# Optimization experiments

Measured on AMD Instinct MI355X. Metric: run time of the kernel, lower is better.

## Reference

```python
import jax, jax.numpy as jnp
import numpy as np

B, L, S = 128, 80, 8          # dialogues, utterances per dialogue, speakers
NODE_DIM, HIDDEN, HEADS, OUT_DIM = 768, 512, 8, 256
N = B * L


def _build_edges():
    """Replicates InterSentenceGNN.build_graph + Batch.from_data_list offsets."""
    rel = np.zeros((N, 3), np.float32)
    all_e, last = [], []
    eye3 = np.eye(3, dtype=np.float32)
    for b in range(B):
        off = b * L
        u = L - 1
        e, t = [], []
        for i in range(L):
            if i > 0:
                e += [[i - 1, i], [i, i - 1]]; t += [0, 0]   # REL_SEQ
            if i < u:
                e += [[i, u], [u, i]]; t += [1, 1]           # REL_CTX
        for s in range(S):                                   # REL_SPK, round-robin speakers
            g = list(range(s, L, S))
            for a in range(len(g)):
                for c in range(a + 1, len(g)):
                    e += [[g[a], g[c]], [g[c], g[a]]]; t += [2, 2]
        e = np.asarray(e, np.int64); t = np.asarray(t, np.int64)
        np.add.at(rel, e[:, 0] + off, eye3[t])               # out-degree per relation (pre-unique)
        all_e.append(np.unique(e, axis=0) + off)             # torch.unique(idx, dim=1)
        last.append(off + u)
    edge_index = np.concatenate(all_e, 0).T.astype(np.int32)  # [2, E], row0=src, row1=dst
    return edge_index, rel, np.asarray(last, np.int32)


def setup_inputs() -> dict:
    key = jax.random.key(0)
    ks = jax.random.split(key, 16)
    edge_index, rel_feat, last_idx = _build_edges()
    g = lambda k, shp, fan: jax.random.normal(k, shp, jnp.float32) * (1.0 / np.sqrt(fan))
    return {
        "x": jax.random.normal(ks[0], (N, NODE_DIM), jnp.float32),
        "rel_feat": jnp.asarray(rel_feat),
        "w1": g(ks[1], (3, 64), 3), "b1": jnp.zeros((64,), jnp.float32),
        "w2": g(ks[2], (64, 1), 64), "b2": jnp.zeros((1,), jnp.float32),
        "Wl1": g(ks[3], (NODE_DIM, HIDDEN), NODE_DIM), "bl1": jnp.zeros((HIDDEN,), jnp.float32),
        "Wr1": g(ks[4], (NODE_DIM, HIDDEN), NODE_DIM), "br1": jnp.zeros((HIDDEN,), jnp.float32),
        "att1": g(ks[5], (HEADS, HIDDEN // HEADS), HIDDEN // HEADS),
        "bias1": jnp.zeros((HIDDEN,), jnp.float32),
        "Wl2": g(ks[6], (HIDDEN, OUT_DIM), HIDDEN), "bl2": jnp.zeros((OUT_DIM,), jnp.float32),
        "Wr2": g(ks[7], (HIDDEN, OUT_DIM), HIDDEN), "br2": jnp.zeros((OUT_DIM,), jnp.float32),
        "att2": g(ks[8], (1, OUT_DIM), OUT_DIM),
        "bias2": jnp.zeros((OUT_DIM,), jnp.float32),
        "ln_g": jnp.ones((OUT_DIM,), jnp.float32), "ln_b": jnp.zeros((OUT_DIM,), jnp.float32),
        "edge_index": jnp.asarray(edge_index),
        "last_idx": jnp.asarray(last_idx),
    }


def _gatv2(x, Wl, bl, Wr, br, att, bias, src, dst, heads, ch, concat):
    """PyG GATv2Conv (eval mode, self-loops already in src/dst)."""
    n = x.shape[0]
    xl = (x @ Wl + bl).reshape(n, heads, ch)   # source transform (messages)
    xr = (x @ Wr + br).reshape(n, heads, ch)   # target transform
    e = jax.nn.leaky_relu(xl[src] + xr[dst], negative_slope=0.2)  # [E,H,C]
    logit = jnp.einsum("ehc,hc->eh", e, att)                      # [E,H]
    m = jax.ops.segment_max(logit, dst, num_segments=n)
    a = jnp.exp(logit - m[dst])
    denom = jax.ops.segment_sum(a, dst, num_segments=n)
    alpha = a / denom[dst]                                        # segment softmax over dst
    msg = (xl[src] * alpha[:, :, None]).reshape(-1, heads * ch)
    out = jax.ops.segment_sum(msg, dst, num_segments=n).reshape(n, heads, ch)
    out = out.reshape(n, heads * ch) if concat else out.mean(axis=1)
    return out + bias


def reference(x, rel_feat, w1, b1, w2, b2, Wl1, bl1, Wr1, br1, att1, bias1,
              Wl2, bl2, Wr2, br2, att2, bias2, ln_g, ln_b, edge_index, last_idx):
    n = x.shape[0]
    loops = jnp.arange(n, dtype=edge_index.dtype)
    src = jnp.concatenate([edge_index[0], loops])  # add_self_loops=True (PyG default)
    dst = jnp.concatenate([edge_index[1], loops])
    w = jax.nn.sigmoid(jax.nn.relu(rel_feat @ w1 + b1) @ w2 + b2)  # [N,1] node gate
    h = x * w
    h = jax.nn.elu(_gatv2(h, Wl1, bl1, Wr1, br1, att1, bias1, src, dst, HEADS, HIDDEN // HEADS, True))
    h = _gatv2(h, Wl2, bl2, Wr2, br2, att2, bias2, src, dst, 1, OUT_DIM, False)
    mu = jnp.mean(h, axis=-1, keepdims=True)
    var = jnp.mean((h - mu) ** 2, axis=-1, keepdims=True)
    h = (h - mu) * jax.lax.rsqrt(var + 1e-5) * ln_g + ln_b
    return h[last_idx]  # x[batch.ptr[1:] - 1]: last (context) node per dialogue
```

## Files before the change

### kernel.cpp

```cpp
#include <hip/hip_runtime.h>
#include <hip/hip_bf16.h>

#define NN 10240
#define LL 80
#define BB 128

typedef _Float16 half8 __attribute__((ext_vector_type(8)));
typedef _Float16 half2v __attribute__((ext_vector_type(2)));
typedef float f32x4 __attribute__((ext_vector_type(4)));

#define GLD16(gptr, lptr)                                                        \
  __builtin_amdgcn_global_load_lds(                                              \
      (const __attribute__((address_space(1))) void*)(gptr),                     \
      (__attribute__((address_space(3))) void*)(lptr), 16, 0, 0)

__device__ __forceinline__ float dot2f(half2v a, half2v b, float c) {
#if __has_builtin(__builtin_amdgcn_fdot2)
  return __builtin_amdgcn_fdot2(a, b, c, false);
#else
  return c + (float)a.x * (float)b.x + (float)a.y * (float)b.y;
#endif
}
__device__ __forceinline__ half2v u2h(unsigned int u) { half2v r; __builtin_memcpy(&r, &u, 4); return r; }
__device__ __forceinline__ unsigned int h2u(half2v h) { unsigned int u; __builtin_memcpy(&u, &h, 4); return u; }
__device__ __forceinline__ unsigned int dupf16(float v) {
  _Float16 hv = (_Float16)v;
  unsigned short u; __builtin_memcpy(&u, &hv, 2);
  return (unsigned int)u * 0x10001u;
}

__global__ __launch_bounds__(256) void prep_all(
    const float* __restrict__ x, const float* __restrict__ rel,
    const float* __restrict__ w1, const float* __restrict__ b1,
    const float* __restrict__ w2, const float* __restrict__ b2,
    const float* __restrict__ Wl1, const float* __restrict__ Wr1,
    const float* __restrict__ Wl2, const float* __restrict__ Wr2,
    const float* __restrict__ bl1, const float* __restrict__ br1,
    const float* __restrict__ att1,
    _Float16* __restrict__ h0, _Float16* __restrict__ Wt1,
    _Float16* __restrict__ Wt2cat,
    float* __restrict__ biasc, _Float16* __restrict__ att_h) {
  __shared__ float tile[32][33];
  int bid = blockIdx.x;
  int tid = threadIdx.x;
  if (bid < NN) {
    int n = bid;
    __shared__ float s_w;
    if (tid < 64) {
      float r0 = rel[n * 3 + 0], r1 = rel[n * 3 + 1], r2 = rel[n * 3 + 2];
      float v = r0 * w1[tid] + r1 * w1[64 + tid] + r2 * w1[128 + tid] + b1[tid];
      v = v > 0.f ? v : 0.f;
      v *= w2[tid];
      for (int d = 32; d; d >>= 1) v += __shfl_down(v, d, 64);
      if (tid == 0) s_w = 1.f / (1.f + __expf(-(v + b2[0])));
    }
    __syncthreads();
    float w = s_w;
    const float* xr = x + (size_t)n * 768;
    _Float16* hr = h0 + (size_t)n * 768;
    for (int c = tid; c < 768; c += 256) hr[c] = (_Float16)(xr[c] * w);
    return;
  }
  int r = bid - NN;
  const float* W;
  _Float16* Wt;
  int K, Nc, bx, by;
  if (r < 384)      { W = Wl1; Wt = Wt1;                          K = 768; Nc = 512; bx = r % 16;       by = r / 16; }
  else if (r < 768) { W = Wr1; Wt = Wt1 + (size_t)512 * 768;      K = 768; Nc = 512; bx = (r-384) % 16; by = (r-384) / 16; }
  else if (r < 896) { W = Wl2; Wt = Wt2cat;                       K = 512; Nc = 256; bx = (r-768) % 8;  by = (r-768) / 8; }
  else if (r < 1024){ W = Wr2; Wt = Wt2cat + (size_t)256 * 512;   K = 512; Nc = 256; bx = (r-896) % 8;  by = (r-896) / 8; }
  else {
    for (int i = tid; i < 1024; i += 256) biasc[i] = (i < 512) ? bl1[i] : br1[i - 512];
    for (int i = tid; i < 512; i += 256) att_h[i] = (_Float16)att1[i];
    return;
  }
  int n0 = bx * 32, k0 = by * 32;
  int c = tid & 31, rr = tid >> 5;
#pragma unroll
  for (int p = 0; p < 4; ++p) {
    int rw = p * 8 + rr;
    tile[rw][c] = W[(size_t)(k0 + rw) * Nc + n0 + c];
  }
  __syncthreads();
#pragma unroll
  for (int p = 0; p < 4; ++p) {
    int rw = p * 8 + rr;
    Wt[(size_t)(n0 + rw) * K + k0 + c] = (_Float16)tile[c][rw];
  }
}

#define PB 66
__global__ __launch_bounds__(512, 8) void gemm1gat1(
    const _Float16* __restrict__ h0, const _Float16* __restrict__ Wt1,
    const float* __restrict__ biasc, const _Float16* __restrict__ att_h,
    const float* __restrict__ bias1, _Float16* __restrict__ h1) {
  __shared__ __align__(16) char smem[39936];
  _Float16* As = (_Float16*)smem;
  _Float16* Bs = (_Float16*)(smem + 15360);
  _Float16* s_xl = (_Float16*)smem;
  _Float16* s_xr = (_Float16*)(smem + 10560);
  float* s_logit = (float*)(smem + 21120);
  unsigned int* s_al = (unsigned int*)(smem + 26304);
  short* s_src   = (short*)(smem + 31488);
  short* s_cnt   = (short*)(smem + 34080);
  float* s_hub   = (float*)(smem + 34240);
  unsigned int* s_hub16 = (unsigned int*)(smem + 34560);
  unsigned int* s_hp = (unsigned int*)(smem + 34880);

  int bx = blockIdx.x;
  int h = bx >> 7, b = bx & 127;
  int base = b * LL;
  int tid = threadIdx.x;
  int wave = tid >> 6, lane = tid & 63;
  int lr = lane & 15, lk = lane >> 4;

  const _Float16* aP = h0;
  if (wave < 5) {
    int c = wave * 64 + lane;
    aP = h0 + (size_t)(base + (c >> 2)) * 768 + (c & 3) * 8;
  }
  int cB = wave * 64 + lane;
  int brow = cB >> 2;
  int wrow = (brow < 64) ? (h * 64 + brow) : (512 + h * 64 + (brow - 64));
  const _Float16* bP = Wt1 + (size_t)wrow * 768 + (cB & 3) * 8;

  f32x4 acc[5] = {};
  for (int it = 0; it < 8; ++it) {
    int k0 = it * 96;
    if (wave < 5) {
      GLD16(aP + k0,      As + wave * 512);
      GLD16(aP + k0 + 32, As + 2560 + wave * 512);
      GLD16(aP + k0 + 64, As + 5120 + wave * 512);
    }
    GLD16(bP + k0,      Bs + wave * 512);
    GLD16(bP + k0 + 32, Bs + 4096 + wave * 512);
    GLD16(bP + k0 + 64, Bs + 8192 + wave * 512);
    __syncthreads();
#pragma unroll
    for (int s3 = 0; s3 < 3; ++s3) {
      half8 bf = *(const half8*)(Bs + s3 * 4096 + (wave * 16 + lr) * 32 + lk * 8);
#pragma unroll
      for (int m = 0; m < 5; ++m) {
        half8 af = *(const half8*)(As + s3 * 2560 + (m * 16 + lr) * 32 + lk * 8);
        acc[m] = __builtin_amdgcn_mfma_f32_16x16x32_f16(af, bf, acc[m], 0, 0, 0);
      }
    }
    __syncthreads();
  }
  {
    int c = wave * 16 + lr;
    bool isxl = c < 64;
    int cc = isxl ? c : c - 64;
    float bb = biasc[(isxl ? 0 : 512) + h * 64 + cc];
    _Float16* dst = isxl ? s_xl : s_xr;
#pragma unroll
    for (int m = 0; m < 5; ++m)
#pragma unroll
      for (int rg = 0; rg < 4; ++rg) {
        int row = m * 16 + lk * 4 + rg;
        dst[row * PB + cc] = (_Float16)(acc[m][rg] + bb);
      }
  }
  if (tid < 79) {
    int d = tid;
    int list[16];
    int c = 0;
    list[c++] = d;
    if (d > 0) list[c++] = d - 1;
    if (d + 1 < 79) list[c++] = d + 1;
    list[c++] = 79;
    for (int j = d & 7; j < 80; j += 8)
      if (j != d && j != 79) list[c++] = j;
    s_cnt[d] = (short)c;
    for (int i = c; i < 16; ++i) list[i] = -1;
#pragma unroll
    for (int i = 0; i < 16; ++i) s_src[i * 81 + d] = (short)list[i];
  }
  __syncthreads();

  const unsigned int* pat = (const unsigned int*)(att_h + h * 64);
  const half2v c02 = {(_Float16)0.2f, (_Float16)0.2f};
  for (int s = tid; s < 1344; s += 512) {
    int d, src;
    bool ishub = s >= 1264;
    if (!ishub) { d = s >> 4; src = s_src[(s & 15) * 81 + d]; }
    else { d = 79; src = s - 1264; }
    int ssrc = src < 0 ? 0 : src;
    const unsigned int* pa = (const unsigned int*)(s_xl + ssrc * PB);
    const unsigned int* pb = (const unsigned int*)(s_xr + d * PB);
    float acc2 = 0.f;
#pragma unroll
    for (int q = 0; q < 16; ++q) {
      unsigned int a0 = pa[2 * q], a1 = pa[2 * q + 1];
      unsigned int b0 = pb[2 * q], b1 = pb[2 * q + 1];
      half2v at0 = u2h(__builtin_amdgcn_readfirstlane(pat[2 * q]));
      half2v at1 = u2h(__builtin_amdgcn_readfirstlane(pat[2 * q + 1]));
      half2v e0 = u2h(a0) + u2h(b0);
      half2v e1 = u2h(a1) + u2h(b1);
      half2v l0 = __builtin_elementwise_max(e0, e0 * c02);
      half2v l1 = __builtin_elementwise_max(e1, e1 * c02);
      acc2 = dot2f(l0, at0, acc2);
      acc2 = dot2f(l1, at1, acc2);
    }
    if (!ishub) s_logit[(s & 15) * 81 + d] = (src < 0) ? -3e38f : acc2;
    else s_hub[src] = acc2;
  }
  __syncthreads();

  if (tid < 79) {
    int d = tid;
    float m = -3e38f, v[16];
#pragma unroll
    for (int i = 0; i < 16; ++i) { v[i] = s_logit[i * 81 + d]; m = fmaxf(m, v[i]); }
    float sum = 0.f;
#pragma unroll
    for (int i = 0; i < 16; ++i) { v[i] = __expf(v[i] - m); sum += v[i]; }
    float inv = 1.f / sum;
#pragma unroll
    for (int i = 0; i < 16; ++i) s_al[i * 81 + d] = dupf16(v[i] * inv);
  } else if (tid >= 448) {
    int l = tid - 448;
    float v0 = s_hub[l];
    float v1 = (l < 16) ? s_hub[64 + l] : -3e38f;
    float m = fmaxf(v0, v1);
    for (int d = 32; d; d >>= 1) m = fmaxf(m, __shfl_xor(m, d, 64));
    float e0 = __expf(v0 - m);
    float e1 = (l < 16) ? __expf(v1 - m) : 0.f;
    float sum = e0 + e1;
    for (int d = 32; d; d >>= 1) sum += __shfl_xor(sum, d, 64);
    float inv = 1.f / sum;
    s_hub16[l] = dupf16(e0 * inv);
    if (l < 16) s_hub16[64 + l] = dupf16(e1 * inv);
  }
  __syncthreads();

  int qw = tid >> 4, l = tid & 15;
  int c0 = l * 4;
#pragma unroll
  for (int k = 0; k < 3; ++k) {
    int d = qw + 32 * k;
    if (d >= 79) continue;
    int cnt = s_cnt[d];
    half2v a0 = {(_Float16)0.f, (_Float16)0.f};
    half2v a1 = a0;
    for (int i = 0; i < cnt; ++i) {
      int src = s_src[i * 81 + d];
      half2v al = u2h(s_al[i * 81 + d]);
      const unsigned int* px = (const unsigned int*)(s_xl + src * PB + c0);
      a0 += al * u2h(px[0]);
      a1 += al * u2h(px[1]);
    }
    float v0 = (float)a0.x + bias1[h * 64 + c0];
    float v1 = (float)a0.y + bias1[h * 64 + c0 + 1];
    float v2 = (float)a1.x + bias1[h * 64 + c0 + 2];
    float v3 = (float)a1.y + bias1[h * 64 + c0 + 3];
    v0 = v0 > 0.f ? v0 : __expf(v0) - 1.f;
    v1 = v1 > 0.f ? v1 : __expf(v1) - 1.f;
    v2 = v2 > 0.f ? v2 : __expf(v2) - 1.f;
    v3 = v3 > 0.f ? v3 : __expf(v3) - 1.f;
    half2v o0 = {(_Float16)v0, (_Float16)v1};
    half2v o1 = {(_Float16)v2, (_Float16)v3};
    uint2 ov = {h2u(o0), h2u(o1)};
    *(uint2*)&h1[(size_t)(base + d) * 512 + h * 64 + c0] = ov;
  }
  if (qw >= 16) {
    int g = qw - 16;
    half2v a0 = {(_Float16)0.f, (_Float16)0.f};
    half2v a1 = a0;
#pragma unroll
    for (int s5 = 0; s5 < 5; ++s5) {
      int src = g * 5 + s5;
      half2v al = u2h(s_hub16[src]);
      const unsigned int* px = (const unsigned int*)(s_xl + src * PB + c0);
      a0 += al * u2h(px[0]);
      a1 += al * u2h(px[1]);
    }
    s_hp[g * 32 + 2 * l] = h2u(a0);
    s_hp[g * 32 + 2 * l + 1] = h2u(a1);
  }
  __syncthreads();
  if (tid < 32) {
    float f0 = 0.f, f1 = 0.f;
#pragma unroll
    for (int g = 0; g < 16; ++g) {
      half2v v = u2h(s_hp[g * 32 + tid]);
      f0 += (float)v.x;
      f1 += (float)v.y;
    }
    int c = tid * 2;
    float v0 = f0 + bias1[h * 64 + c];
    float v1 = f1 + bias1[h * 64 + c + 1];
    v0 = v0 > 0.f ? v0 : __expf(v0) - 1.f;
    v1 = v1 > 0.f ? v1 : __expf(v1) - 1.f;
    half2v o = {(_Float16)v0, (_Float16)v1};
    *(unsigned int*)&h1[(size_t)(base + 79) * 512 + h * 64 + c] = h2u(o);
  }
}

#define PX 266
__global__ __launch_bounds__(512) void gemm2gat2(
    const _Float16* __restrict__ h1, const _Float16* __restrict__ Bt,
    const float* __restrict__ bl2, const float* __restrict__ br2,
    const float* __restrict__ att2, const float* __restrict__ bias2,
    const float* __restrict__ ln_g, const float* __restrict__ ln_b,
    float* __restrict__ out) {
  __shared__ __align__(16) char smem[80 * PX * 2];
  __shared__ _Float16 s_att[256];
  __shared__ _Float16 s_xr[256];
  __shared__ float s_red[80];
  __shared__ float s_sum[4], s_sq[4];
  _Float16* As = (_Float16*)smem;
  _Float16* Bs = (_Float16*)(smem + 5120);
  _Float16* s_x = (_Float16*)smem;

  int b = blockIdx.x;
  int tid = threadIdx.x;
  int wave = tid >> 6, lane = tid & 63;
  int lr = lane & 15, lk = lane >> 4;

  if (tid < 256) s_att[tid] = (_Float16)att2[tid];

  int achunk = wave * 64 + lane;
  const _Float16* aP = h1 + (size_t)(b * 80 + (achunk >> 2)) * 512 + (achunk & 3) * 8;
  const _Float16* bP[4];
#pragma unroll
  for (int j = 0; j < 4; ++j) {
    int c = wave * 256 + j * 64 + lane;
    bP[j] = Bt + (size_t)(c >> 2) * 512 + (c & 3) * 8;
  }
  f32x4 acc[5][4] = {};
  for (int k0 = 0; k0 < 512; k0 += 32) {
    if (wave < 5) GLD16(aP + k0, As + wave * 512);
#pragma unroll
    for (int j = 0; j < 4; ++j)
      GLD16(bP[j] + k0, Bs + (wave * 256 + j * 64) * 8);
    __syncthreads();
    half8 af[5], bfv;
#pragma unroll
    for (int i = 0; i < 5; ++i)
      af[i] = *(const half8*)(As + (i * 16 + lr) * 32 + lk * 8);
#pragma unroll
    for (int j = 0; j < 4; ++j) {
      bfv = *(const half8*)(Bs + (wave * 64 + j * 16 + lr) * 32 + lk * 8);
#pragma unroll
      for (int i = 0; i < 5; ++i)
        acc[i][j] = __builtin_amdgcn_mfma_f32_16x16x32_f16(af[i], bfv, acc[i][j], 0, 0, 0);
    }
    __syncthreads();
  }
  if (wave < 4) {
#pragma unroll
    for (int i = 0; i < 5; ++i)
#pragma unroll
      for (int j = 0; j < 4; ++j)
#pragma unroll
        for (int rg = 0; rg < 4; ++rg) {
          int row = i * 16 + lk * 4 + rg;
          int col = wave * 64 + j * 16 + lr;
          s_x[row * PX + col] = (_Float16)(acc[i][j][rg] + bl2[col]);
        }
  } else if (lk == 3) {
#pragma unroll
    for (int j = 0; j < 4; ++j) {
      int colx = (wave - 4) * 64 + j * 16 + lr;
      s_xr[colx] = (_Float16)(acc[4][j][3] + br2[colx]);
    }
  }
  __syncthreads();
  if (tid < 160) {
    int r = tid >> 1, hf = tid & 1;
    const half2v* xa = (const half2v*)(s_x + r * PX + hf * 128);
    const half2v* xr = (const half2v*)(s_xr + hf * 128);
    const half2v* at = (const half2v*)(s_att + hf * 128);
    float lg = 0.f;
    const half2v c02 = {(_Float16)0.2f, (_Float16)0.2f};
#pragma unroll
    for (int q = 0; q < 64; ++q) {
      half2v e = xa[q] + xr[q];
      half2v l = __builtin_elementwise_max(e, e * c02);
      lg = dot2f(l, at[q], lg);
    }
    lg += __shfl_xor(lg, 1, 64);
    if (hf == 0) s_red[r] = lg;
  }
  __syncthreads();
  if (wave == 7) {
    float v0 = s_red[lane];
    float v1 = (lane < 16) ? s_red[64 + lane] : -3e38f;
    float m = fmaxf(v0, v1);
    for (int d = 32; d; d >>= 1) m = fmaxf(m, __shfl_xor(m, d, 64));
    float e0 = __expf(v0 - m);
    float e1 = (lane < 16) ? __expf(v1 - m) : 0.f;
    float sum = e0 + e1;
    for (int d = 32; d; d >>= 1) sum += __shfl_xor(sum, d, 64);
    float inv = 1.f / sum;
    s_red[lane] = e0 * inv;
    if (lane < 16) s_red[64 + lane] = e1 * inv;
  }
  __syncthreads();
  float v = 0.f;
  if (tid < 256) {
    float a = 0.f;
#pragma unroll
    for (int r = 0; r < 80; ++r) a += s_red[r] * (float)s_x[r * PX + tid];
    v = a + bias2[tid];
    float p = v;
    for (int d = 32; d; d >>= 1) p += __shfl_down(p, d, 64);
    if (lane == 0) s_sum[wave] = p;
    float q = v * v;
    for (int d = 32; d; d >>= 1) q += __shfl_down(q, d, 64);
    if (lane == 0) s_sq[wave] = q;
  }
  __syncthreads();
  if (tid < 256) {
    float mu = (s_sum[0] + s_sum[1] + s_sum[2] + s_sum[3]) * (1.f / 256.f);
    float ex2 = (s_sq[0] + s_sq[1] + s_sq[2] + s_sq[3]) * (1.f / 256.f);
    float var = ex2 - mu * mu;
    float r = rsqrtf(var + 1e-5f);
    out[b * 256 + tid] = (v - mu) * r * ln_g[tid] + ln_b[tid];
  }
}

extern "C" void kernel_launch(void* const* d_in, const int* in_sizes, int n_in,
                              void* d_out, int out_size, void* d_ws, size_t ws_size,
                              hipStream_t stream) {
  const float* x      = (const float*)d_in[0];
  const float* rel    = (const float*)d_in[1];
  const float* w1     = (const float*)d_in[2];
  const float* b1     = (const float*)d_in[3];
  const float* w2     = (const float*)d_in[4];
  const float* b2     = (const float*)d_in[5];
  const float* Wl1    = (const float*)d_in[6];
  const float* bl1    = (const float*)d_in[7];
  const float* Wr1    = (const float*)d_in[8];
  const float* br1    = (const float*)d_in[9];
  const float* att1   = (const float*)d_in[10];
  const float* bias1  = (const float*)d_in[11];
  const float* Wl2    = (const float*)d_in[12];
  const float* bl2    = (const float*)d_in[13];
  const float* Wr2    = (const float*)d_in[14];
  const float* br2    = (const float*)d_in[15];
  const float* att2   = (const float*)d_in[16];
  const float* bias2  = (const float*)d_in[17];
  const float* ln_g   = (const float*)d_in[18];
  const float* ln_b   = (const float*)d_in[19];
  float* out = (float*)d_out;

  char* p = (char*)d_ws;
  _Float16* h0     = (_Float16*)p; p += (size_t)NN * 768 * 2;
  _Float16* h1     = (_Float16*)p; p += (size_t)NN * 512 * 2;
  _Float16* Wt1    = (_Float16*)p; p += (size_t)1024 * 768 * 2;
  _Float16* Wt2cat = (_Float16*)p; p += (size_t)512 * 512 * 2;
  _Float16* att_h  = (_Float16*)p; p += 1024;
  float* biasc     = (float*)p; p += 1024 * 4;

  prep_all<<<NN + 1025, 256, 0, stream>>>(x, rel, w1, b1, w2, b2, Wl1, Wr1, Wl2, Wr2,
                                          bl1, br1, att1, h0, Wt1, Wt2cat, biasc, att_h);

  gemm1gat1<<<1024, 512, 0, stream>>>(h0, Wt1, biasc, att_h, bias1, h1);

  gemm2gat2<<<BB, 512, 0, stream>>>(h1, Wt2cat, bl2, br2, att2, bias2, ln_g, ln_b, out);
}
```

Measured before the change: 190.7 us.

## Split GEMM1 K-loop across wave groups with LDS partial-sum reduction

Restructures the fused GEMM1+GAT1 kernel so that the 8 waves form two K-split groups. Each wave now computes a 32-column by 80-row tile, so one B-fragment load feeds five MFMAs and one A-fragment load feeds two. The loop runs 12 steps of 64-wide K instead of 8 steps of 96. The upper group's partial sums are packed to fp16 and reduced through LDS into the lower group. The xl/xr row stride is also padded every 8 rows to cut LDS bank conflicts. In exchange there are more loop iterations with barriers, an extra reduction pass, and some precision loss from storing partials in fp16.

```diff
diff --git a/kernel.cpp b/kernel.cpp
--- a/kernel.cpp
+++ b/kernel.cpp
@@ -28,6 +28,7 @@
   unsigned short u; __builtin_memcpy(&u, &hv, 2);
   return (unsigned int)u * 0x10001u;
 }
+__device__ __forceinline__ int roff(int r) { return r * 66 + 2 * (r >> 3); }
 
 __global__ __launch_bounds__(256) void prep_all(
     const float* __restrict__ x, const float* __restrict__ rel,
@@ -89,23 +90,23 @@
   }
 }
 
-#define PB 66
 __global__ __launch_bounds__(512, 8) void gemm1gat1(
     const _Float16* __restrict__ h0, const _Float16* __restrict__ Wt1,
     const float* __restrict__ biasc, const _Float16* __restrict__ att_h,
     const float* __restrict__ bias1, _Float16* __restrict__ h1) {
-  __shared__ __align__(16) char smem[39936];
+  __shared__ __align__(16) char smem[37056];
   _Float16* As = (_Float16*)smem;
-  _Float16* Bs = (_Float16*)(smem + 15360);
+  _Float16* Bs = (_Float16*)(smem + 10240);
+  unsigned int* red = (unsigned int*)smem;
   _Float16* s_xl = (_Float16*)smem;
-  _Float16* s_xr = (_Float16*)(smem + 10560);
-  float* s_logit = (float*)(smem + 21120);
-  unsigned int* s_al = (unsigned int*)(smem + 26304);
-  short* s_src   = (short*)(smem + 31488);
-  short* s_cnt   = (short*)(smem + 34080);
-  float* s_hub   = (float*)(smem + 34240);
-  unsigned int* s_hub16 = (unsigned int*)(smem + 34560);
-  unsigned int* s_hp = (unsigned int*)(smem + 34880);
+  _Float16* s_xr = (_Float16*)(smem + 10624);
+  float* s_logit = (float*)(smem + 21248);
+  unsigned int* s_al = (unsigned int*)(smem + 26432);
+  short* s_src   = (short*)(smem + 31616);
+  short* s_cnt   = (short*)(smem + 34208);
+  float* s_hub   = (float*)(smem + 34368);
+  unsigned int* s_hub16 = (unsigned int*)(smem + 34688);
+  unsigned int* s_hp = (unsigned int*)(smem + 35008);
 
   int bx = blockIdx.x;
   int h = bx >> 7, b = bx & 127;
@@ -113,53 +114,86 @@
   int tid = threadIdx.x;
   int wave = tid >> 6, lane = tid & 63;
   int lr = lane & 15, lk = lane >> 4;
+  int g = wave >> 2, np = wave & 3;
 
   const _Float16* aP = h0;
   if (wave < 5) {
-    int c = wave * 64 + lane;
-    aP = h0 + (size_t)(base + (c >> 2)) * 768 + (c & 3) * 8;
-  }
-  int cB = wave * 64 + lane;
-  int brow = cB >> 2;
+    aP = h0 + (size_t)(base + (tid >> 2)) * 768 + (tid & 3) * 8;
+  }
+  int brow = tid >> 2;
   int wrow = (brow < 64) ? (h * 64 + brow) : (512 + h * 64 + (brow - 64));
-  const _Float16* bP = Wt1 + (size_t)wrow * 768 + (cB & 3) * 8;
-
-  f32x4 acc[5] = {};
-  for (int it = 0; it < 8; ++it) {
-    int k0 = it * 96;
+  const _Float16* bP = Wt1 + (size_t)wrow * 768 + (tid & 3) * 8;
+
+  f32x4 acc[5][2] = {};
+  const _Float16* bbase = Bs + g * 4096 + (np * 32 + lr) * 32 + lk * 8;
+  const _Float16* abase = As + g * 2560 + lr * 32 + lk * 8;
+  for (int it = 0; it < 12; ++it) {
+    int k0 = it * 64;
     if (wave < 5) {
-      GLD16(aP + k0,      As + wave * 512);
-      GLD16(aP + k0 + 32, As + 2560 + wave * 512);
-      GLD16(aP + k0 + 64, As + 5120 + wave * 512);
-    }
-    GLD16(bP + k0,      Bs + wave * 512);
-    GLD16(bP + k0 + 32, Bs + 4096 + wave * 512);
-    GLD16(bP + k0 + 64, Bs + 8192 + wave * 512);
+      GLD16(aP + k0,      As + tid * 8);
+      GLD16(aP + k0 + 32, As + 2560 + tid * 8);
+    }
+    GLD16(bP + k0,      Bs + tid * 8);
+    GLD16(bP + k0 + 32, Bs + 4096 + tid * 8);
     __syncthreads();
-#pragma unroll
-    for (int s3 = 0; s3 < 3; ++s3) {
-      half8 bf = *(const half8*)(Bs + s3 * 4096 + (wave * 16 + lr) * 32 + lk * 8);
-#pragma unroll
-      for (int m = 0; m < 5; ++m) {
-        half8 af = *(const half8*)(As + s3 * 2560 + (m * 16 + lr) * 32 + lk * 8);
-        acc[m] = __builtin_amdgcn_mfma_f32_16x16x32_f16(af, bf, acc[m], 0, 0, 0);
+    half8 bf0 = *(const half8*)(bbase);
+    half8 bf1 = *(const half8*)(bbase + 512);
+#pragma unroll
+    for (int m = 0; m < 5; ++m) {
+      half8 af = *(const half8*)(abase + m * 512);
+      acc[m][0] = __builtin_amdgcn_mfma_f32_16x16x32_f16(af, bf0, acc[m][0], 0, 0, 0);
+      acc[m][1] = __builtin_amdgcn_mfma_f32_16x16x32_f16(af, bf1, acc[m][1], 0, 0, 0);
+    }
+    __syncthreads();
+  }
+  if (wave >= 4) {
+#pragma unroll
+    for (int m = 0; m < 5; ++m)
+#pragma unroll
+      for (int s = 0; s < 2; ++s) {
+        int col = np * 32 + s * 16 + lr;
+        int rbase = col * 41 + 8 * m + 2 * lk;
+#pragma unroll
+        for (int rp = 0; rp < 2; ++rp) {
+          half2v pv = {(_Float16)acc[m][s][2 * rp], (_Float16)acc[m][s][2 * rp + 1]};
+          red[rbase + rp] = h2u(pv);
+        }
       }
-    }
-    __syncthreads();
-  }
-  {
-    int c = wave * 16 + lr;
-    bool isxl = c < 64;
-    int cc = isxl ? c : c - 64;
-    float bb = biasc[(isxl ? 0 : 512) + h * 64 + cc];
-    _Float16* dst = isxl ? s_xl : s_xr;
+  }
+  __syncthreads();
+  if (wave < 4) {
 #pragma unroll
     for (int m = 0; m < 5; ++m)
 #pragma unroll
-      for (int rg = 0; rg < 4; ++rg) {
-        int row = m * 16 + lk * 4 + rg;
-        dst[row * PB + cc] = (_Float16)(acc[m][rg] + bb);
+      for (int s = 0; s < 2; ++s) {
+        int col = np * 32 + s * 16 + lr;
+        int rbase = col * 41 + 8 * m + 2 * lk;
+#pragma unroll
+        for (int rp = 0; rp < 2; ++rp) {
+          half2v pv = u2h(red[rbase + rp]);
+          acc[m][s][2 * rp] += (float)pv.x;
+          acc[m][s][2 * rp + 1] += (float)pv.y;
+        }
       }
+  }
+  __syncthreads();
+
+  if (wave < 4) {
+#pragma unroll
+    for (int s = 0; s < 2; ++s) {
+      int col = np * 32 + s * 16 + lr;
+      bool isxl = col < 64;
+      int cc = isxl ? col : col - 64;
+      float bb = biasc[(isxl ? 0 : 512) + h * 64 + cc];
+      _Float16* dst = isxl ? s_xl : s_xr;
+#pragma unroll
+      for (int m = 0; m < 5; ++m)
+#pragma unroll
+        for (int rg = 0; rg < 4; ++rg) {
+          int row = m * 16 + lk * 4 + rg;
+          dst[roff(row) + cc] = (_Float16)(acc[m][s][rg] + bb);
+        }
+    }
   }
   if (tid < 79) {
     int d = tid;
@@ -186,8 +220,8 @@
     if (!ishub) { d = s >> 4; src = s_src[(s & 15) * 81 + d]; }
     else { d = 79; src = s - 1264; }
     int ssrc = src < 0 ? 0 : src;
-    const unsigned int* pa = (const unsigned int*)(s_xl + ssrc * PB);
-    const unsigned int* pb = (const unsigned int*)(s_xr + d * PB);
+    const unsigned int* pa = (const unsigned int*)(s_xl + roff(ssrc));
+    const unsigned int* pb = (const unsigned int*)(s_xr + roff(d));
     float acc2 = 0.f;
 #pragma unroll
     for (int q = 0; q < 16; ++q) {
@@ -246,7 +280,7 @@
     for (int i = 0; i < cnt; ++i) {
       int src = s_src[i * 81 + d];
       half2v al = u2h(s_al[i * 81 + d]);
-      const unsigned int* px = (const unsigned int*)(s_xl + src * PB + c0);
+      const unsigned int* px = (const unsigned int*)(s_xl + roff(src) + c0);
       a0 += al * u2h(px[0]);
       a1 += al * u2h(px[1]);
     }
@@ -264,26 +298,26 @@
     *(uint2*)&h1[(size_t)(base + d) * 512 + h * 64 + c0] = ov;
   }
   if (qw >= 16) {
-    int g = qw - 16;
+    int gg = qw - 16;
     half2v a0 = {(_Float16)0.f, (_Float16)0.f};
     half2v a1 = a0;
 #pragma unroll
     for (int s5 = 0; s5 < 5; ++s5) {
-      int src = g * 5 + s5;
+      int src = gg * 5 + s5;
       half2v al = u2h(s_hub16[src]);
-      const unsigned int* px = (const unsigned int*)(s_xl + src * PB + c0);
+      const unsigned int* px = (const unsigned int*)(s_xl + roff(src) + c0);
       a0 += al * u2h(px[0]);
       a1 += al * u2h(px[1]);
     }
-    s_hp[g * 32 + 2 * l] = h2u(a0);
-    s_hp[g * 32 + 2 * l + 1] = h2u(a1);
+    s_hp[gg * 32 + 2 * l] = h2u(a0);
+    s_hp[gg * 32 + 2 * l + 1] = h2u(a1);
   }
   __syncthreads();
   if (tid < 32) {
     float f0 = 0.f, f1 = 0.f;
 #pragma unroll
-    for (int g = 0; g < 16; ++g) {
-      half2v v = u2h(s_hp[g * 32 + tid]);
+    for (int gg = 0; gg < 16; ++gg) {
+      half2v v = u2h(s_hp[gg * 32 + tid]);
       f0 += (float)v.x;
       f1 += (float)v.y;
     }
```

After: 195.4 us. 1.02x slower.
